# Kernel optimization log

Measured on AMD Instinct MI355X. Metric: run time of the kernel, lower is better.

## Reference

```python
import jax, jax.numpy as jnp
import numpy as np

N = 200            # dihedral parameter, group order 2N per copy -> reg rep dim 2N=400
IN_C, OUT_C = 32, 32
GENERATORS = [(0, 1), (1, 0), (0, 3), (1, 5)]


def _dihedral_perm(n, a, b):
    """2n x 2n permutation matrix of the regular representation (right action)."""
    i = np.arange(n)
    P_rot = np.zeros((2 * n, 2 * n), dtype=np.float32)
    P_rot[i, (i + b) % n] = 1.0
    P_rot[i + n, n + (i + b) % n] = 1.0
    if a == 0:
        return P_rot
    P_refl = np.zeros((2 * n, 2 * n), dtype=np.float32)
    P_refl[i, n + (-i) % n] = 1.0
    P_refl[i + n, (-i) % n] = 1.0
    return (P_rot @ P_refl).astype(np.float32)


def setup_inputs() -> dict:
    key = jax.random.key(0)
    kx, kw = jax.random.split(key)
    x = jax.random.normal(kx, (512, IN_C, 2 * N), dtype=jnp.float32)
    # kaiming-uniform-like init for weight [G, in, out]
    fan_in = IN_C
    bound = float(np.sqrt(6.0 / ((1 + 2.0) * fan_in)))
    weight = jax.random.uniform(kw, (len(GENERATORS), IN_C, OUT_C),
                                dtype=jnp.float32, minval=-bound, maxval=bound)
    perm = jnp.asarray(np.stack([_dihedral_perm(N, a, b) for a, b in GENERATORS]))
    return {"x": x, "weight": weight, "perm": perm}


def reference(x, weight, perm):
    # filter[c,i,d,o] = sum_g perm[g,i,o] * weight[g,c,d]
    B = x.shape[0]
    two_n = perm.shape[1]
    filt = jnp.einsum('gio,gcd->cido', perm, weight)
    filt = filt.reshape(IN_C * two_n, OUT_C * two_n)
    out = x.reshape(B, -1) @ filt          # [B, out_c*2n]
    return out.reshape(B, OUT_C, two_n)
```

## Files before the change

### kernel.cpp

```cpp
#include <hip/hip_runtime.h>

#define TWO_N 400
#define IN_C 32
#define OUT_C 32
#define NG 4
#define NB 512
#define K_TOT 128

typedef __attribute__((ext_vector_type(8))) short bf16x8;
typedef __attribute__((ext_vector_type(4))) float f32x4;

static __device__ inline unsigned short f2bf(float f) {
    unsigned u = __float_as_uint(f);
    u = (u + 0x7FFFu + ((u >> 16) & 1u)) >> 16;
    return (unsigned short)u;
}

#define WS_WT_OFF   8192
#define WS_XT_OFF   32768

__global__ __launch_bounds__(256) void prep_kernel(
        const float* __restrict__ x, const float* __restrict__ w,
        const float* __restrict__ perm,
        int* __restrict__ inv_t, unsigned short* __restrict__ wt,
        unsigned short* __restrict__ xt) {
    const int blk = blockIdx.x;
    const int t   = threadIdx.x;

    if (blk < 800) {
        int tid = blk * 256 + t;
        int b = tid / TWO_N;
        int i = tid - b * TWO_N;
        const float* xb = x + (size_t)b * IN_C * TWO_N + i;
        unsigned pk[16];
#pragma unroll
        for (int c2 = 0; c2 < 16; ++c2) {
            float v0 = xb[(size_t)(2 * c2) * TWO_N];
            float v1 = xb[(size_t)(2 * c2 + 1) * TWO_N];
            pk[c2] = (unsigned)f2bf(v0) | ((unsigned)f2bf(v1) << 16);
        }
        uint4* dst = (uint4*)(xt + (size_t)tid * 32);
#pragma unroll
        for (int j = 0; j < 4; ++j) {
            uint4 u = {pk[4 * j], pk[4 * j + 1], pk[4 * j + 2], pk[4 * j + 3]};
            dst[j] = u;
        }
    } else if (blk < 3300) {
        int tt = (blk - 800) * 256 + t;
        float v = perm[tt];
        if (v > 0.5f) {
            int g = tt / (TWO_N * TWO_N);
            int rem = tt - g * (TWO_N * TWO_N);
            int i = rem / TWO_N;
            int o = rem - i * TWO_N;
            inv_t[o * 4 + g] = i;
        }
    } else {
        int f = (blk - 3300) * 256 + t;
        int d = f & 31;
        int c = (f >> 5) & 31;
        int g = f >> 10;
        wt[d * K_TOT + g * 32 + c] = f2bf(w[f]);
    }
}

__global__ __launch_bounds__(256) void dihedral_conv_mfma(
        const int* __restrict__ inv_t,
        const unsigned short* __restrict__ wt,
        const unsigned short* __restrict__ xt,
        float* __restrict__ out) {
    const int b    = blockIdx.x;
    const int lane = threadIdx.x & 63;
    const int wid  = threadIdx.x >> 6;
    const int l15  = lane & 15;
    const int q    = lane >> 4;

    bf16x8 afrag[2][4];
#pragma unroll
    for (int dt = 0; dt < 2; ++dt)
#pragma unroll
        for (int g = 0; g < NG; ++g)
            afrag[dt][g] = *(const bf16x8*)(wt + (dt * 16 + l15) * K_TOT
                                               + g * 32 + q * 8);

    const unsigned short* xb = xt + (size_t)b * (TWO_N * IN_C);
    float* outb = out + (size_t)b * (OUT_C * TWO_N);

    int ot = wid;
    int4 iv = *(const int4*)(inv_t + (ot * 16 + l15) * 4);
    while (true) {
        int ot_n = ot + 4;
        bool has_n = (ot_n < 25);
        int4 iv_n;
        if (has_n)
            iv_n = *(const int4*)(inv_t + (ot_n * 16 + l15) * 4);

        bf16x8 b0 = *(const bf16x8*)(xb + iv.x * IN_C + q * 8);
        bf16x8 b1 = *(const bf16x8*)(xb + iv.y * IN_C + q * 8);
        bf16x8 b2 = *(const bf16x8*)(xb + iv.z * IN_C + q * 8);
        bf16x8 b3 = *(const bf16x8*)(xb + iv.w * IN_C + q * 8);

        f32x4 acc0 = {0.f, 0.f, 0.f, 0.f};
        f32x4 acc1 = {0.f, 0.f, 0.f, 0.f};
        acc0 = __builtin_amdgcn_mfma_f32_16x16x32_bf16(afrag[0][0], b0, acc0, 0, 0, 0);
        acc1 = __builtin_amdgcn_mfma_f32_16x16x32_bf16(afrag[1][0], b0, acc1, 0, 0, 0);
        acc0 = __builtin_amdgcn_mfma_f32_16x16x32_bf16(afrag[0][1], b1, acc0, 0, 0, 0);
        acc1 = __builtin_amdgcn_mfma_f32_16x16x32_bf16(afrag[1][1], b1, acc1, 0, 0, 0);
        acc0 = __builtin_amdgcn_mfma_f32_16x16x32_bf16(afrag[0][2], b2, acc0, 0, 0, 0);
        acc1 = __builtin_amdgcn_mfma_f32_16x16x32_bf16(afrag[1][2], b2, acc1, 0, 0, 0);
        acc0 = __builtin_amdgcn_mfma_f32_16x16x32_bf16(afrag[0][3], b3, acc0, 0, 0, 0);
        acc1 = __builtin_amdgcn_mfma_f32_16x16x32_bf16(afrag[1][3], b3, acc1, 0, 0, 0);

        float* op0 = outb + (size_t)(q * 4) * TWO_N + ot * 16 + l15;
        float* op1 = op0 + (size_t)16 * TWO_N;
#pragma unroll
        for (int j = 0; j < 4; ++j) {
            __builtin_nontemporal_store(acc0[j], op0 + (size_t)j * TWO_N);
            __builtin_nontemporal_store(acc1[j], op1 + (size_t)j * TWO_N);
        }

        if (!has_n) break;
        ot = ot_n;
        iv = iv_n;
    }
}

extern "C" void kernel_launch(void* const* d_in, const int* in_sizes, int n_in,
                              void* d_out, int out_size, void* d_ws, size_t ws_size,
                              hipStream_t stream) {
    const float* x    = (const float*)d_in[0];
    const float* w    = (const float*)d_in[1];
    const float* perm = (const float*)d_in[2];
    float* out = (float*)d_out;

    char* ws = (char*)d_ws;
    int*            inv_t = (int*)ws;
    unsigned short* wt    = (unsigned short*)(ws + WS_WT_OFF);
    unsigned short* xt    = (unsigned short*)(ws + WS_XT_OFF);

    prep_kernel<<<3316, 256, 0, stream>>>(x, w, perm, inv_t, wt, xt);
    dihedral_conv_mfma<<<NB, 256, 0, stream>>>(inv_t, wt, xt, out);
}
```

Baseline: 90.09 us.

## Split x transpose and conv output tiles across four times more blocks

```diff
diff --git a/kernel.cpp b/kernel.cpp
--- a/kernel.cpp
+++ b/kernel.cpp
@@ -27,26 +27,25 @@
     const int blk = blockIdx.x;
     const int t   = threadIdx.x;
 
-    if (blk < 800) {
+    if (blk < 3200) {
         int tid = blk * 256 + t;
-        int b = tid / TWO_N;
-        int i = tid - b * TWO_N;
+        int row = tid >> 2;
+        int cb  = (tid & 3) * 8;
+        int b = row / TWO_N;
+        int i = row - b * TWO_N;
         const float* xb = x + (size_t)b * IN_C * TWO_N + i;
-        unsigned pk[16];
+        float v[8];
 #pragma unroll
-        for (int c2 = 0; c2 < 16; ++c2) {
-            float v0 = xb[(size_t)(2 * c2) * TWO_N];
-            float v1 = xb[(size_t)(2 * c2 + 1) * TWO_N];
-            pk[c2] = (unsigned)f2bf(v0) | ((unsigned)f2bf(v1) << 16);
-        }
-        uint4* dst = (uint4*)(xt + (size_t)tid * 32);
+        for (int j = 0; j < 8; ++j)
+            v[j] = xb[(size_t)(cb + j) * TWO_N];
+        unsigned pk[4];
 #pragma unroll
-        for (int j = 0; j < 4; ++j) {
-            uint4 u = {pk[4 * j], pk[4 * j + 1], pk[4 * j + 2], pk[4 * j + 3]};
-            dst[j] = u;
-        }
-    } else if (blk < 3300) {
-        int tt = (blk - 800) * 256 + t;
+        for (int k = 0; k < 4; ++k)
+            pk[k] = (unsigned)f2bf(v[2 * k]) | ((unsigned)f2bf(v[2 * k + 1]) << 16);
+        uint4 u = {pk[0], pk[1], pk[2], pk[3]};
+        *(uint4*)(xt + (size_t)tid * 8) = u;
+    } else if (blk < 5700) {
+        int tt = (blk - 3200) * 256 + t;
         float v = perm[tt];
         if (v > 0.5f) {
             int g = tt / (TWO_N * TWO_N);
@@ -56,7 +55,7 @@
             inv_t[o * 4 + g] = i;
         }
     } else {
-        int f = (blk - 3300) * 256 + t;
+        int f = (blk - 5700) * 256 + t;
         int d = f & 31;
         int c = (f >> 5) & 31;
         int g = f >> 10;
@@ -69,11 +68,14 @@
         const unsigned short* __restrict__ wt,
         const unsigned short* __restrict__ xt,
         float* __restrict__ out) {
-    const int b    = blockIdx.x;
+    const int blk  = blockIdx.x;
+    const int b    = blk >> 2;
+    const int part = blk & 3;
     const int lane = threadIdx.x & 63;
     const int wid  = threadIdx.x >> 6;
     const int l15  = lane & 15;
     const int q    = lane >> 4;
+    const int s    = part * 4 + wid;
 
     bf16x8 afrag[2][4];
 #pragma unroll
@@ -86,14 +88,8 @@
     const unsigned short* xb = xt + (size_t)b * (TWO_N * IN_C);
     float* outb = out + (size_t)b * (OUT_C * TWO_N);
 
-    int ot = wid;
-    int4 iv = *(const int4*)(inv_t + (ot * 16 + l15) * 4);
-    while (true) {
-        int ot_n = ot + 4;
-        bool has_n = (ot_n < 25);
-        int4 iv_n;
-        if (has_n)
-            iv_n = *(const int4*)(inv_t + (ot_n * 16 + l15) * 4);
+    for (int T = s; T < 25; T += 16) {
+        int4 iv = *(const int4*)(inv_t + (T * 16 + l15) * 4);
 
         bf16x8 b0 = *(const bf16x8*)(xb + iv.x * IN_C + q * 8);
         bf16x8 b1 = *(const bf16x8*)(xb + iv.y * IN_C + q * 8);
@@ -111,17 +107,13 @@
         acc0 = __builtin_amdgcn_mfma_f32_16x16x32_bf16(afrag[0][3], b3, acc0, 0, 0, 0);
         acc1 = __builtin_amdgcn_mfma_f32_16x16x32_bf16(afrag[1][3], b3, acc1, 0, 0, 0);
 
-        float* op0 = outb + (size_t)(q * 4) * TWO_N + ot * 16 + l15;
+        float* op0 = outb + (size_t)(q * 4) * TWO_N + T * 16 + l15;
         float* op1 = op0 + (size_t)16 * TWO_N;
 #pragma unroll
         for (int j = 0; j < 4; ++j) {
             __builtin_nontemporal_store(acc0[j], op0 + (size_t)j * TWO_N);
             __builtin_nontemporal_store(acc1[j], op1 + (size_t)j * TWO_N);
         }
-
-        if (!has_n) break;
-        ot = ot_n;
-        iv = iv_n;
     }
 }
 
@@ -138,6 +130,6 @@
     unsigned short* wt    = (unsigned short*)(ws + WS_WT_OFF);
     unsigned short* xt    = (unsigned short*)(ws + WS_XT_OFF);
 
-    prep_kernel<<<3316, 256, 0, stream>>>(x, w, perm, inv_t, wt, xt);
-    dihedral_conv_mfma<<<NB, 256, 0, stream>>>(inv_t, wt, xt, out);
+    prep_kernel<<<5716, 256, 0, stream>>>(x, w, perm, inv_t, wt, xt);
+    dihedral_conv_mfma<<<NB * 4, 256, 0, stream>>>(inv_t, wt, xt, out);
 }
```

Measured after the change: 95.99 us. 1.07x slower.
